# Performance work log

Measured on AMD Instinct MI355X. Metric: run time of the kernel, lower is better.

The kernel has to match this reference:

```python
import jax, jax.numpy as jnp
import numpy as np
import math

NUM_HEADS = 16
THETA = 10000.0


def _rope(x, token_pos, theta):
    # x: [B, H, S, d_k]; token_pos: [S]
    d_k = x.shape[-1]
    freqs = 1.0 / theta ** (jnp.arange(0, d_k, 2, dtype=jnp.float32) / d_k)  # [d_k/2]
    angles = token_pos.astype(jnp.float32)[:, None] * freqs[None, :]         # [S, d_k/2]
    cos, sin = jnp.cos(angles), jnp.sin(angles)
    x1 = x[..., 0::2]
    x2 = x[..., 1::2]
    out1 = x1 * cos - x2 * sin
    out2 = x1 * sin + x2 * cos
    # interleave back: (..., d_k/2, 2) -> (..., d_k)
    return jnp.stack([out1, out2], axis=-1).reshape(x.shape)


def setup_inputs() -> dict:
    key = jax.random.key(0)
    ks = jax.random.split(key, 5)
    B, S, D = 4, 2048, 1024
    scale = 0.02
    return {
        "x": jax.random.normal(ks[0], (B, S, D), dtype=jnp.float32),
        "token_pos": jnp.arange(S, dtype=jnp.int64 if jax.config.jax_enable_x64 else jnp.int32),
        "Wq": jax.random.normal(ks[1], (D, D), dtype=jnp.float32) * scale,
        "Wk": jax.random.normal(ks[2], (D, D), dtype=jnp.float32) * scale,
        "Wv": jax.random.normal(ks[3], (D, D), dtype=jnp.float32) * scale,
        "Wo": jax.random.normal(ks[4], (D, D), dtype=jnp.float32) * scale,
    }


def reference(x, token_pos, Wq, Wk, Wv, Wo):
    B, S, D = x.shape
    H = NUM_HEADS
    d_k = D // H
    # projections (Linear without bias: y = x @ W^T, W is [out, in])
    def proj(W):
        y = jnp.einsum('bsd,ed->bse', x, W)
        return y.reshape(B, S, H, d_k).transpose(0, 2, 1, 3)  # [B,H,S,d_k]
    q, k, v = proj(Wq), proj(Wk), proj(Wv)
    q = _rope(q, token_pos, THETA)
    k = _rope(k, token_pos, THETA)
    scores = jnp.einsum('bhqd,bhkd->bhqk', q, k) / math.sqrt(d_k)
    causal = jnp.tril(jnp.ones((S, S), dtype=bool))
    scores = jnp.where(causal, scores, -jnp.inf)
    attn = jax.nn.softmax(scores, axis=-1)
    out = jnp.einsum('bhqk,bhkd->bhqd', attn, v)            # [B,H,S,d_k]
    out = out.transpose(0, 2, 1, 3).reshape(B, S, D)
    return jnp.einsum('bsd,ed->bse', out, Wo)
```

## Files before the change

kernel.cpp:

```cpp
#include <hip/hip_runtime.h>

typedef unsigned short u16;
typedef __bf16 bf16x8 __attribute__((ext_vector_type(8)));
typedef float f32x4 __attribute__((ext_vector_type(4)));
typedef u16 u16x8 __attribute__((ext_vector_type(8)));

#define B_ 4
#define S_ 2048
#define D_ 1024
#define H_ 16
#define LOG2E 1.44269504f

__device__ inline u16 f2bf(float f) {
  unsigned u = __float_as_uint(f);
  u = u + 0x7fffu + ((u >> 16) & 1u);
  return (u16)(u >> 16);
}
__device__ inline u16 f2bf_hw(float f) {
  __bf16 b = (__bf16)f;
  return __builtin_bit_cast(u16, b);
}
__device__ inline float bf2f(u16 h) {
  return __uint_as_float(((unsigned)h) << 16);
}
__device__ inline void gload_lds16(const u16* g, u16* l) {
  __builtin_amdgcn_global_load_lds((const __attribute__((address_space(1))) void*)g,
                                   (__attribute__((address_space(3))) void*)l, 16, 0, 0);
}
__device__ inline float fast_exp2(float x) {
  float r;
  asm("v_exp_f32 %0, %1" : "=v"(r) : "v"(x));
  return r;
}

__global__ __launch_bounds__(256) void k_prep(const float* __restrict__ x,
                                              const float* __restrict__ w0,
                                              const float* __restrict__ w1,
                                              const float* __restrict__ w2,
                                              const float* __restrict__ w3,
                                              const int* __restrict__ pos,
                                              u16* __restrict__ xb,
                                              u16* __restrict__ wdst,
                                              float2* __restrict__ tab) {
  const int bid = blockIdx.x;
  if (bid < 8192) {
    int i = bid * 256 + threadIdx.x;
    float4 v = reinterpret_cast<const float4*>(x)[i];
    ushort4 o;
    o.x = f2bf(v.x); o.y = f2bf(v.y); o.z = f2bf(v.z); o.w = f2bf(v.w);
    reinterpret_cast<ushort4*>(xb)[i] = o;
  } else if (bid < 12288) {
    int i = (bid - 8192) * 256 + threadIdx.x;
    const int tensor = i >> 18;
    const int local = i & 262143;
    const float* s = tensor == 0 ? w0 : tensor == 1 ? w1 : tensor == 2 ? w2 : w3;
    float4 v = reinterpret_cast<const float4*>(s)[local];
    ushort4 o;
    o.x = f2bf(v.x); o.y = f2bf(v.y); o.z = f2bf(v.z); o.w = f2bf(v.w);
    reinterpret_cast<ushort4*>(wdst + (size_t)tensor * 1048576)[local] = o;
  } else {
    int idx = (bid - 12288) * 256 + threadIdx.x;
    int s = idx >> 5, i = idx & 31;
    float freq = powf(10000.0f, -(float)i * (1.0f / 32.0f));
    float ang = (float)pos[s] * freq;
    float sn, c;
    sincosf(ang, &sn, &c);
    tab[idx] = make_float2(c, sn);
  }
}

__global__ __launch_bounds__(256) void k_rope_k(u16* __restrict__ kb,
                                                const float2* __restrict__ tab) {
  int idx = blockIdx.x * 256 + threadIdx.x;
  const int row = idx >> 7;
  const int s = row & 2047;
  const int chunk = idx & 127;
  u16* p = kb + ((size_t)row << 10) + chunk * 8;
  u16x8 v = *reinterpret_cast<u16x8*>(p);
  const float4* tp = reinterpret_cast<const float4*>(tab + s * 32 + (chunk & 7) * 4);
  float4 t0 = tp[0], t1 = tp[1];
  float cc[4] = {t0.x, t0.z, t1.x, t1.z};
  float ss[4] = {t0.y, t0.w, t1.y, t1.w};
  u16x8 o;
#pragma unroll
  for (int u = 0; u < 4; u++) {
    float x1 = bf2f(v[2 * u]), x2 = bf2f(v[2 * u + 1]);
    o[2 * u]     = f2bf(x1 * cc[u] - x2 * ss[u]);
    o[2 * u + 1] = f2bf(x1 * ss[u] + x2 * cc[u]);
  }
  *reinterpret_cast<u16x8*>(p) = o;
}

__global__ __launch_bounds__(256) void k_gemm_qkv(const u16* __restrict__ A,
                                                  const u16* __restrict__ Bcat,
                                                  u16* __restrict__ Ccat,
                                                  u16* __restrict__ Vt) {
  __shared__ u16 As[2][128 * 64];
  __shared__ u16 Bs[2][128 * 64];
  const int K = 1024;
  const int xcd = blockIdx.x & 7;
  const int idx = blockIdx.x >> 3;
  const int st = idx >> 6;
  const int mi = (idx & 63) >> 3;
  const int ni = idx & 7;
  const int by = xcd * 8 + mi;
  const int bx = st * 8 + ni;
  const int m0 = by << 7, n0 = bx << 7;
  const int tid = threadIdx.x;
  const int lane = tid & 63;
  const int wv = tid >> 6;
  const int wm = (wv >> 1) << 6;
  const int wn = (wv & 1) << 6;
  const int r = lane & 15, g = lane >> 4;

  f32x4 acc[4][4] = {};

  const int srow0 = tid >> 3;
  const int scol = (((tid & 7) ^ ((tid >> 3) & 7)) * 8);
  const int csw = r & 7;

  const u16* Ab = A + (size_t)(m0 + srow0) * K + scol;
  const u16* Bb = Bcat + (size_t)(n0 + srow0) * K + scol;

#define STAGEQ(k0v, bf) do {                                       \
    const u16* a_ = Ab + (k0v);                                    \
    const u16* b_ = Bb + (k0v);                                    \
    gload_lds16(a_,                &As[bf][0] + tid * 8);          \
    gload_lds16(a_ + (size_t)32 * K, &As[bf][0] + tid * 8 + 2048); \
    gload_lds16(a_ + (size_t)64 * K, &As[bf][0] + tid * 8 + 4096); \
    gload_lds16(a_ + (size_t)96 * K, &As[bf][0] + tid * 8 + 6144); \
    gload_lds16(b_,                &Bs[bf][0] + tid * 8);          \
    gload_lds16(b_ + (size_t)32 * K, &Bs[bf][0] + tid * 8 + 2048); \
    gload_lds16(b_ + (size_t)64 * K, &Bs[bf][0] + tid * 8 + 4096); \
    gload_lds16(b_ + (size_t)96 * K, &Bs[bf][0] + tid * 8 + 6144); \
  } while (0)

  STAGEQ(0, 0);

  for (int t = 0; t < 16; ++t) {
    const int bsel = t & 1;
    if (t < 15) {
      STAGEQ((t + 1) * 64, bsel ^ 1);
      asm volatile("s_waitcnt vmcnt(8)" ::: "memory");
    } else {
      asm volatile("s_waitcnt vmcnt(0)" ::: "memory");
    }
    __builtin_amdgcn_s_barrier();
    asm volatile("" ::: "memory");

#pragma unroll
    for (int ks = 0; ks < 2; ks++) {
      bf16x8 af[4], bfr[4];
#pragma unroll
      for (int i = 0; i < 4; i++)
        af[i] = *reinterpret_cast<const bf16x8*>(
            &As[bsel][(wm + i * 16 + r) * 64 + (((ks * 4 + g) ^ csw) * 8)]);
#pragma unroll
      for (int t2 = 0; t2 < 4; t2++)
        bfr[t2] = *reinterpret_cast<const bf16x8*>(
            &Bs[bsel][(wn + t2 * 16 + r) * 64 + (((ks * 4 + g) ^ csw) * 8)]);
#pragma unroll
      for (int i = 0; i < 4; i++)
#pragma unroll
        for (int t2 = 0; t2 < 4; t2++)
          acc[i][t2] = __builtin_amdgcn_mfma_f32_16x16x32_bf16(af[i], bfr[t2], acc[i][t2], 0, 0, 0);
    }
    asm volatile("" ::: "memory");
    __builtin_amdgcn_s_barrier();
  }
#undef STAGEQ

  const int bq = n0 >> 10;
  const int c0 = n0 & 1023;
  if (bq == 2) {
#pragma unroll
    for (int i = 0; i < 4; i++) {
#pragma unroll
      for (int t = 0; t < 4; t++) {
        const int row = m0 + wm + i * 16 + g * 4;
        const int col = c0 + wn + t * 16 + r;
        const int b = row >> 11, s0 = row & 2047;
        const int h = col >> 6, d = col & 63;
        ushort4 o;
        o.x = f2bf(acc[i][t][0]); o.y = f2bf(acc[i][t][1]);
        o.z = f2bf(acc[i][t][2]); o.w = f2bf(acc[i][t][3]);
        *reinterpret_cast<ushort4*>(
            Vt + (((size_t)(b * 16 + h) * 64 + d) << 11) + s0) = o;
      }
    }
  } else {
    u16* Cb = Ccat + (size_t)bq * (8192 * 1024);
#pragma unroll
    for (int i = 0; i < 4; i++) {
#pragma unroll
      for (int t = 0; t < 4; t++) {
        const int row = m0 + wm + i * 16 + g * 4;
        const int col = c0 + wn + t * 16 + r;
#pragma unroll
        for (int j = 0; j < 4; j++)
          Cb[(size_t)(row + j) * 1024 + col] = f2bf(acc[i][t][j]);
      }
    }
  }
}

__global__ __launch_bounds__(256) void k_gemm_bt(const u16* __restrict__ A,
                                                 const u16* __restrict__ Bw,
                                                 float* __restrict__ C,
                                                 int M, int N, int K) {
  __shared__ u16 As[2][128 * 64];
  __shared__ u16 Bs[2][128 * 64];
  const int nbx = N >> 7;
  const int swz = (blockIdx.x & 7) * (gridDim.x >> 3) + (blockIdx.x >> 3);
  const int bx = swz % nbx;
  const int by = swz / nbx;
  const int m0 = by << 7, n0 = bx << 7;
  const int tid = threadIdx.x;
  const int lane = tid & 63;
  const int wv = tid >> 6;
  const int wm = (wv >> 1) << 6;
  const int wn = (wv & 1) << 6;
  const int r = lane & 15, g = lane >> 4;

  f32x4 acc[4][4] = {};

  const int srow0 = tid >> 3;
  const int scol = (((tid & 7) ^ ((tid >> 3) & 7)) * 8);
  const int csw = r & 7;

  const u16* Ab = A + (size_t)(m0 + srow0) * K + scol;
  const u16* Bb = Bw + (size_t)(n0 + srow0) * K + scol;
  const int nt = K >> 6;

#define STAGEW(k0v, bf) do {                                       \
    const u16* a_ = Ab + (k0v);                                    \
    const u16* b_ = Bb + (k0v);                                    \
    gload_lds16(a_,                &As[bf][0] + tid * 8);          \
    gload_lds16(a_ + (size_t)32 * K, &As[bf][0] + tid * 8 + 2048); \
    gload_lds16(a_ + (size_t)64 * K, &As[bf][0] + tid * 8 + 4096); \
    gload_lds16(a_ + (size_t)96 * K, &As[bf][0] + tid * 8 + 6144); \
    gload_lds16(b_,                &Bs[bf][0] + tid * 8);          \
    gload_lds16(b_ + (size_t)32 * K, &Bs[bf][0] + tid * 8 + 2048); \
    gload_lds16(b_ + (size_t)64 * K, &Bs[bf][0] + tid * 8 + 4096); \
    gload_lds16(b_ + (size_t)96 * K, &Bs[bf][0] + tid * 8 + 6144); \
  } while (0)

  STAGEW(0, 0);

  for (int t = 0; t < nt; ++t) {
    const int bsel = t & 1;
    if (t < nt - 1) {
      STAGEW((t + 1) * 64, bsel ^ 1);
      asm volatile("s_waitcnt vmcnt(8)" ::: "memory");
    } else {
      asm volatile("s_waitcnt vmcnt(0)" ::: "memory");
    }
    __builtin_amdgcn_s_barrier();
    asm volatile("" ::: "memory");

#pragma unroll
    for (int ks = 0; ks < 2; ks++) {
      bf16x8 af[4], bfr[4];
#pragma unroll
      for (int i = 0; i < 4; i++)
        af[i] = *reinterpret_cast<const bf16x8*>(
            &As[bsel][(wm + i * 16 + r) * 64 + (((ks * 4 + g) ^ csw) * 8)]);
#pragma unroll
      for (int t2 = 0; t2 < 4; t2++)
        bfr[t2] = *reinterpret_cast<const bf16x8*>(
            &Bs[bsel][(wn + t2 * 16 + r) * 64 + (((ks * 4 + g) ^ csw) * 8)]);
#pragma unroll
      for (int i = 0; i < 4; i++)
#pragma unroll
        for (int t2 = 0; t2 < 4; t2++)
          acc[i][t2] = __builtin_amdgcn_mfma_f32_16x16x32_bf16(af[i], bfr[t2], acc[i][t2], 0, 0, 0);
    }
    asm volatile("" ::: "memory");
    __builtin_amdgcn_s_barrier();
  }
#undef STAGEW

#pragma unroll
  for (int i = 0; i < 4; i++) {
#pragma unroll
    for (int t = 0; t < 4; t++) {
      const int row = m0 + wm + i * 16 + g * 4;
      const int col = n0 + wn + t * 16 + r;
#pragma unroll
      for (int j = 0; j < 4; j++)
        C[(size_t)(row + j) * N + col] = acc[i][t][j];
    }
  }
}

__global__ __launch_bounds__(256) void k_attn14(const u16* __restrict__ Q,
                                                const u16* __restrict__ Kb,
                                                const u16* __restrict__ Vt,
                                                const float2* __restrict__ tab,
                                                u16* __restrict__ O) {
  __shared__ u16 Ks[64 * 64];
  __shared__ u16 Vs[64 * 64];
  __shared__ u16 Ps[4][32 * 64];

  const int bh = (blockIdx.x & 7) * 8 + ((blockIdx.x >> 3) & 7);
  const int qt = 15 - (blockIdx.x >> 6);
  const int b = bh >> 4, h = bh & 15;
  const int tid = threadIdx.x;
  const int lane = tid & 63, w = tid >> 6;
  const int g = lane >> 4, r = lane & 15;

  const u16* Kbase = Kb + (size_t)(b * S_) * 1024 + h * 64;
  const u16* Vbase = Vt + (size_t)bh * 64 * 2048;

  const int srow = tid >> 3;
  const int scol = ((tid & 7) * 8) ^ ((srow & 7) * 8);
  const int rsw = (r & 7) * 8;

  const int qbase = qt << 7;
  const int qrow0 = qbase + (w << 5);

  const float QSC = 0.125f * LOG2E;
  bf16x8 qf[2][2];
#pragma unroll
  for (int f = 0; f < 2; f++) {
    const int s = qrow0 + f * 16 + r;
    const u16* qrow = Q + (size_t)(b * S_ + s) * 1024 + h * 64;
    qf[f][0] = *reinterpret_cast<const bf16x8*>(qrow + g * 8);
    qf[f][1] = *reinterpret_cast<const bf16x8*>(qrow + 32 + g * 8);
    const float4* tp = reinterpret_cast<const float4*>(tab + s * 32);
#pragma unroll
    for (int c = 0; c < 2; c++) {
      float4 t0 = tp[c * 8 + g * 2], t1 = tp[c * 8 + g * 2 + 1];
      float cc[4] = {t0.x, t0.z, t1.x, t1.z};
      float ss[4] = {t0.y, t0.w, t1.y, t1.w};
      bf16x8 q = qf[f][c];
#pragma unroll
      for (int u = 0; u < 4; u++) {
        float x1 = (float)q[2 * u], x2 = (float)q[2 * u + 1];
        q[2 * u]     = (__bf16)((x1 * cc[u] - x2 * ss[u]) * QSC);
        q[2 * u + 1] = (__bf16)((x1 * ss[u] + x2 * cc[u]) * QSC);
      }
      qf[f][c] = q;
    }
  }

  bf16x8 ones;
#pragma unroll
  for (int u = 0; u < 8; u++) ones[u] = (__bf16)1.0f;

  f32x4 o_acc[2][4] = {};
  f32x4 lacc[2] = {};
  u16* pb0 = &Ps[w][r * 64];
  u16* pb1 = &Ps[w][(16 + r) * 64];

  const u16* kp0 = Kbase + (size_t)srow * 1024 + scol;
  const u16* kp1 = kp0 + 32 * 1024;
  const u16* vp0 = Vbase + (size_t)srow * 2048 + scol;
  const u16* vp1 = vp0 + 32 * 2048;

  const int kend = qbase + 128;
  for (int k0 = 0; k0 < kend; k0 += 64) {
    gload_lds16(kp0, Ks + tid * 8);
    gload_lds16(kp1, Ks + tid * 8 + 2048);
    gload_lds16(vp0, Vs + tid * 8);
    gload_lds16(vp1, Vs + tid * 8 + 2048);
    kp0 += 64 * 1024; kp1 += 64 * 1024; vp0 += 64; vp1 += 64;
    __syncthreads();

    if (k0 <= qrow0 + 31) {
      const int rem0 = qrow0 + 15 - k0;
      const int rem1 = qrow0 + 31 - k0;
      const int ktlim0 = rem0 < 0 ? 0 : (rem0 >= 48 ? 4 : (rem0 >> 4) + 1);
      const int ktlim1 = rem1 >= 48 ? 4 : (rem1 >> 4) + 1;
      const bool mask0 = (k0 + 63 > qrow0);
      const bool mask1 = (k0 + 63 > qrow0 + 16);

#pragma unroll
      for (int kt = 0; kt < 4; kt++) {
        const int pc = (kt * 16 + g * 4) ^ rsw;
        if (kt >= ktlim1) {
          ushort4 z = {0, 0, 0, 0};
          *reinterpret_cast<ushort4*>(pb0 + pc) = z;
          *reinterpret_cast<ushort4*>(pb1 + pc) = z;
          continue;
        }
        const int krow = kt * 16 + r;
        bf16x8 kf0 = *reinterpret_cast<const bf16x8*>(&Ks[krow * 64 + ((g * 8) ^ rsw)]);
        bf16x8 kf1 = *reinterpret_cast<const bf16x8*>(&Ks[krow * 64 + ((32 + g * 8) ^ rsw)]);
        f32x4 s0 = {}, s1 = {};
        if (kt < ktlim0) {
          s0 = __builtin_amdgcn_mfma_f32_16x16x32_bf16(kf0, qf[0][0], s0, 0, 0, 0);
          s0 = __builtin_amdgcn_mfma_f32_16x16x32_bf16(kf1, qf[0][1], s0, 0, 0, 0);
        }
        s1 = __builtin_amdgcn_mfma_f32_16x16x32_bf16(kf0, qf[1][0], s1, 0, 0, 0);
        s1 = __builtin_amdgcn_mfma_f32_16x16x32_bf16(kf1, qf[1][1], s1, 0, 0, 0);

        const int colb = k0 + kt * 16 + g * 4;
        float p0[4], p1[4];
        if (kt < ktlim0) {
          if (mask0) {
#pragma unroll
            for (int j = 0; j < 4; j++)
              if (colb + j > qrow0 + r) s0[j] = -1e30f;
          }
#pragma unroll
          for (int j = 0; j < 4; j++) p0[j] = fast_exp2(s0[j]);
        } else {
#pragma unroll
          for (int j = 0; j < 4; j++) p0[j] = 0.f;
        }
        if (mask1) {
#pragma unroll
          for (int j = 0; j < 4; j++)
            if (colb + j > qrow0 + 16 + r) s1[j] = -1e30f;
        }
#pragma unroll
        for (int j = 0; j < 4; j++) p1[j] = fast_exp2(s1[j]);

        ushort4 w0, w1;
        w0.x = f2bf_hw(p0[0]); w0.y = f2bf_hw(p0[1]); w0.z = f2bf_hw(p0[2]); w0.w = f2bf_hw(p0[3]);
        w1.x = f2bf_hw(p1[0]); w1.y = f2bf_hw(p1[1]); w1.z = f2bf_hw(p1[2]); w1.w = f2bf_hw(p1[3]);
        *reinterpret_cast<ushort4*>(pb0 + pc) = w0;
        *reinterpret_cast<ushort4*>(pb1 + pc) = w1;
      }
      asm volatile("s_waitcnt lgkmcnt(0)" ::: "memory");

#pragma unroll
      for (int kc = 0; kc < 2; kc++) {
        const int cb = (kc * 32 + g * 8) ^ rsw;
        bf16x8 pf0 = *reinterpret_cast<const bf16x8*>(pb0 + cb);
        bf16x8 pf1 = *reinterpret_cast<const bf16x8*>(pb1 + cb);
        lacc[0] = __builtin_amdgcn_mfma_f32_16x16x32_bf16(pf0, ones, lacc[0], 0, 0, 0);
        lacc[1] = __builtin_amdgcn_mfma_f32_16x16x32_bf16(pf1, ones, lacc[1], 0, 0, 0);
#pragma unroll
        for (int dt = 0; dt < 4; dt++) {
          bf16x8 vf = *reinterpret_cast<const bf16x8*>(
              &Vs[(dt * 16 + r) * 64 + ((kc * 32 + g * 8) ^ rsw)]);
          o_acc[0][dt] = __builtin_amdgcn_mfma_f32_16x16x32_bf16(pf0, vf, o_acc[0][dt], 0, 0, 0);
          o_acc[1][dt] = __builtin_amdgcn_mfma_f32_16x16x32_bf16(pf1, vf, o_acc[1][dt], 0, 0, 0);
        }
      }
    }
    __syncthreads();
  }

#pragma unroll
  for (int f = 0; f < 2; f++) {
    u16* orow = O + (size_t)(b * S_ + qrow0 + f * 16) * 1024 + h * 64;
#pragma unroll
    for (int j = 0; j < 4; j++) {
      const float rln = 1.0f / lacc[f][j];
#pragma unroll
      for (int dt = 0; dt < 4; dt++)
        orow[(size_t)(g * 4 + j) * 1024 + dt * 16 + r] = f2bf(o_acc[f][dt][j] * rln);
    }
  }
}

extern "C" void kernel_launch(void* const* d_in, const int* in_sizes, int n_in,
                              void* d_out, int out_size, void* d_ws, size_t ws_size,
                              hipStream_t stream) {
  const float* x  = (const float*)d_in[0];
  const int*   pos = (const int*)d_in[1];
  const float* Wq = (const float*)d_in[2];
  const float* Wk = (const float*)d_in[3];
  const float* Wv = (const float*)d_in[4];
  const float* Wo = (const float*)d_in[5];
  float* out = (float*)d_out;

  char* ws = (char*)d_ws;
  size_t off = 0;
  auto alloc = [&](size_t bytes) {
    void* p = ws + off;
    off += (bytes + 255) & ~(size_t)255;
    return p;
  };
  const size_t XB = (size_t)8192 * 1024 * 2;
  u16* xb  = (u16*)alloc(XB);
  u16* wqb = (u16*)alloc((size_t)1024 * 1024 * 2);
  u16* wkb = (u16*)alloc((size_t)1024 * 1024 * 2);
  u16* wvb = (u16*)alloc((size_t)1024 * 1024 * 2);
  u16* wob = (u16*)alloc((size_t)1024 * 1024 * 2);
  u16* qb  = (u16*)alloc(XB);
  u16* kb  = (u16*)alloc(XB);
  u16* ob  = (u16*)alloc(XB);
  u16* vt  = (u16*)alloc(XB);
  float2* tab = (float2*)alloc((size_t)2048 * 32 * sizeof(float2));
  (void)wkb; (void)wvb;

  k_prep<<<12544, 256, 0, stream>>>(x, Wq, Wk, Wv, Wo, pos, xb, wqb, tab);

  k_gemm_qkv<<<1536, 256, 0, stream>>>(xb, wqb, qb, vt);

  k_rope_k<<<4096, 256, 0, stream>>>(kb, tab);

  k_attn14<<<1024, 256, 0, stream>>>(qb, kb, vt, tab, ob);

  k_gemm_bt<<<512, 256, 0, stream>>>(ob, wob, out, 8192, 1024, 1024);
}
```

Baseline: 171.6 us.

## Widen QKV GEMM tile to 128x256 and drop double-buffered LDS pipeline

The QKV projection GEMM now computes 128x256 output tiles per block, with each wave holding a 64x128 accumulator. The grid is halved and the block-to-tile mapping is rewritten. The double-buffered async-load pipeline with explicit vmcnt waits is replaced by a single-buffered loop that loads and then syncs, so global loads no longer overlap with MFMA work. The aim is more arithmetic per loaded byte and fewer blocks, at the cost of exposed load latency, higher register pressure (128 accumulator floats per thread), and possibly lower occupancy.

Result: slower. 197.2 us (+14.9%).

```diff
diff --git a/kernel.cpp b/kernel.cpp
--- a/kernel.cpp
+++ b/kernel.cpp
@@ -95,25 +95,23 @@
                                                   const u16* __restrict__ Bcat,
                                                   u16* __restrict__ Ccat,
                                                   u16* __restrict__ Vt) {
-  __shared__ u16 As[2][128 * 64];
-  __shared__ u16 Bs[2][128 * 64];
+  __shared__ u16 As[128 * 64];
+  __shared__ u16 Bs[256 * 64];
   const int K = 1024;
   const int xcd = blockIdx.x & 7;
   const int idx = blockIdx.x >> 3;
-  const int st = idx >> 6;
-  const int mi = (idx & 63) >> 3;
-  const int ni = idx & 7;
-  const int by = xcd * 8 + mi;
-  const int bx = st * 8 + ni;
-  const int m0 = by << 7, n0 = bx << 7;
+  const int win = idx >> 5;
+  const int by = xcd * 8 + ((idx >> 2) & 7);
+  const int bx = win * 4 + (idx & 3);
+  const int m0 = by << 7, n0 = bx << 8;
   const int tid = threadIdx.x;
   const int lane = tid & 63;
   const int wv = tid >> 6;
   const int wm = (wv >> 1) << 6;
-  const int wn = (wv & 1) << 6;
+  const int wn = (wv & 1) << 7;
   const int r = lane & 15, g = lane >> 4;
 
-  f32x4 acc[4][4] = {};
+  f32x4 acc[4][8] = {};
 
   const int srow0 = tid >> 3;
   const int scol = (((tid & 7) ^ ((tid >> 3) & 7)) * 8);
@@ -122,53 +120,34 @@
   const u16* Ab = A + (size_t)(m0 + srow0) * K + scol;
   const u16* Bb = Bcat + (size_t)(n0 + srow0) * K + scol;
 
-#define STAGEQ(k0v, bf) do {                                       \
-    const u16* a_ = Ab + (k0v);                                    \
-    const u16* b_ = Bb + (k0v);                                    \
-    gload_lds16(a_,                &As[bf][0] + tid * 8);          \
-    gload_lds16(a_ + (size_t)32 * K, &As[bf][0] + tid * 8 + 2048); \
-    gload_lds16(a_ + (size_t)64 * K, &As[bf][0] + tid * 8 + 4096); \
-    gload_lds16(a_ + (size_t)96 * K, &As[bf][0] + tid * 8 + 6144); \
-    gload_lds16(b_,                &Bs[bf][0] + tid * 8);          \
-    gload_lds16(b_ + (size_t)32 * K, &Bs[bf][0] + tid * 8 + 2048); \
-    gload_lds16(b_ + (size_t)64 * K, &Bs[bf][0] + tid * 8 + 4096); \
-    gload_lds16(b_ + (size_t)96 * K, &Bs[bf][0] + tid * 8 + 6144); \
-  } while (0)
-
-  STAGEQ(0, 0);
-
-  for (int t = 0; t < 16; ++t) {
-    const int bsel = t & 1;
-    if (t < 15) {
-      STAGEQ((t + 1) * 64, bsel ^ 1);
-      asm volatile("s_waitcnt vmcnt(8)" ::: "memory");
-    } else {
-      asm volatile("s_waitcnt vmcnt(0)" ::: "memory");
-    }
-    __builtin_amdgcn_s_barrier();
-    asm volatile("" ::: "memory");
+  for (int k0 = 0; k0 < K; k0 += 64) {
+#pragma unroll
+    for (int i = 0; i < 4; i++)
+      gload_lds16(Ab + k0 + (size_t)(32 * i) * K, As + tid * 8 + i * 2048);
+#pragma unroll
+    for (int i = 0; i < 8; i++)
+      gload_lds16(Bb + k0 + (size_t)(32 * i) * K, Bs + tid * 8 + i * 2048);
+    __syncthreads();
 
 #pragma unroll
     for (int ks = 0; ks < 2; ks++) {
-      bf16x8 af[4], bfr[4];
+      bf16x8 af[4], bfr[8];
 #pragma unroll
       for (int i = 0; i < 4; i++)
         af[i] = *reinterpret_cast<const bf16x8*>(
-            &As[bsel][(wm + i * 16 + r) * 64 + (((ks * 4 + g) ^ csw) * 8)]);
-#pragma unroll
-      for (int t2 = 0; t2 < 4; t2++)
+            &As[(wm + i * 16 + r) * 64 + (((ks * 4 + g) ^ csw) * 8)]);
+#pragma unroll
+      for (int t2 = 0; t2 < 8; t2++)
         bfr[t2] = *reinterpret_cast<const bf16x8*>(
-            &Bs[bsel][(wn + t2 * 16 + r) * 64 + (((ks * 4 + g) ^ csw) * 8)]);
+            &Bs[(wn + t2 * 16 + r) * 64 + (((ks * 4 + g) ^ csw) * 8)]);
 #pragma unroll
       for (int i = 0; i < 4; i++)
 #pragma unroll
-        for (int t2 = 0; t2 < 4; t2++)
+        for (int t2 = 0; t2 < 8; t2++)
           acc[i][t2] = __builtin_amdgcn_mfma_f32_16x16x32_bf16(af[i], bfr[t2], acc[i][t2], 0, 0, 0);
     }
-    asm volatile("" ::: "memory");
-    __builtin_amdgcn_s_barrier();
-  }
-#undef STAGEQ
+    __syncthreads();
+  }
 
   const int bq = n0 >> 10;
   const int c0 = n0 & 1023;
@@ -176,7 +155,7 @@
 #pragma unroll
     for (int i = 0; i < 4; i++) {
 #pragma unroll
-      for (int t = 0; t < 4; t++) {
+      for (int t = 0; t < 8; t++) {
         const int row = m0 + wm + i * 16 + g * 4;
         const int col = c0 + wn + t * 16 + r;
         const int b = row >> 11, s0 = row & 2047;
@@ -193,7 +172,7 @@
 #pragma unroll
     for (int i = 0; i < 4; i++) {
 #pragma unroll
-      for (int t = 0; t < 4; t++) {
+      for (int t = 0; t < 8; t++) {
         const int row = m0 + wm + i * 16 + g * 4;
         const int col = c0 + wn + t * 16 + r;
 #pragma unroll
@@ -490,7 +469,7 @@
 
   k_prep<<<12544, 256, 0, stream>>>(x, Wq, Wk, Wv, Wo, pos, xb, wqb, tab);
 
-  k_gemm_qkv<<<1536, 256, 0, stream>>>(xb, wqb, qb, vt);
+  k_gemm_qkv<<<768, 256, 0, stream>>>(xb, wqb, qb, vt);
 
   k_rope_k<<<4096, 256, 0, stream>>>(kb, tab);
 
```

## Split fused QKV GEMM into 256x256-tile QK GEMM and separate V GEMM

Applied to the files above, without the earlier changes.

Replaces the single 128x128-tile QKV projection kernel with two launches. Q and K are computed by a new 512-thread kernel using 256x256 tiles, which gives more data reuse per LDS load and fewer blocks. V is computed by its own 128x128 kernel that writes the transposed layout. This adds an extra launch and a tail effect (256 blocks on 256 CUs, one wave) in exchange for higher arithmetic intensity on the QK part. It also doubles LDS per block (64KB) and raises register pressure from 32 accumulator tiles per wave.

Result: faster. 167.2 us (median of 3 runs) (-2.6%).

```diff
diff --git a/kernel.cpp b/kernel.cpp
--- a/kernel.cpp
+++ b/kernel.cpp
@@ -91,20 +91,103 @@
   *reinterpret_cast<u16x8*>(p) = o;
 }
 
-__global__ __launch_bounds__(256) void k_gemm_qkv(const u16* __restrict__ A,
-                                                  const u16* __restrict__ Bcat,
-                                                  u16* __restrict__ Ccat,
-                                                  u16* __restrict__ Vt) {
+__global__ __launch_bounds__(512) void k_gemm_qk(const u16* __restrict__ A,
+                                                 const u16* __restrict__ Bqk,
+                                                 u16* __restrict__ Cqk) {
+  __shared__ u16 As[2][256 * 64];
+  __shared__ u16 Bs[2][256 * 64];
+  const int K = 1024;
+  const int xcd = blockIdx.x & 7;
+  const int idx = blockIdx.x >> 3;
+  const int by = xcd * 4 + (idx & 3);
+  const int bx = idx >> 2;
+  const int m0 = by << 8, n0 = bx << 8;
+  const int tid = threadIdx.x;
+  const int lane = tid & 63, w = tid >> 6;
+  const int wr = w >> 2, wc = w & 3;
+  const int r = lane & 15, g = lane >> 4;
+
+  f32x4 acc[8][4] = {};
+
+  const int srow = tid >> 3;
+  const int scol = (((tid & 7) ^ ((tid >> 3) & 7)) * 8);
+  const int csw = r & 7;
+
+  const u16* Ab = A + (size_t)(m0 + srow) * K + scol;
+  const u16* Bb = Bqk + (size_t)(n0 + srow) * K + scol;
+
+#define STG(k0v, bf) do {                                                \
+    gload_lds16(Ab + (k0v),                   &As[bf][0] + tid * 8);     \
+    gload_lds16(Ab + (k0v) + (size_t)64 * K,  &As[bf][0] + tid * 8 + 4096);  \
+    gload_lds16(Ab + (k0v) + (size_t)128 * K, &As[bf][0] + tid * 8 + 8192);  \
+    gload_lds16(Ab + (k0v) + (size_t)192 * K, &As[bf][0] + tid * 8 + 12288); \
+    gload_lds16(Bb + (k0v),                   &Bs[bf][0] + tid * 8);     \
+    gload_lds16(Bb + (k0v) + (size_t)64 * K,  &Bs[bf][0] + tid * 8 + 4096);  \
+    gload_lds16(Bb + (k0v) + (size_t)128 * K, &Bs[bf][0] + tid * 8 + 8192);  \
+    gload_lds16(Bb + (k0v) + (size_t)192 * K, &Bs[bf][0] + tid * 8 + 12288); \
+  } while (0)
+
+  STG(0, 0);
+
+  for (int t = 0; t < 16; ++t) {
+    const int bsel = t & 1;
+    if (t < 15) {
+      STG((t + 1) * 64, bsel ^ 1);
+      asm volatile("s_waitcnt vmcnt(8)" ::: "memory");
+    } else {
+      asm volatile("s_waitcnt vmcnt(0)" ::: "memory");
+    }
+    __builtin_amdgcn_s_barrier();
+    asm volatile("" ::: "memory");
+
+    const u16* Ah = &As[bsel][(wr * 128) * 64];
+    const u16* Bh = &Bs[bsel][(wc * 64) * 64];
+#pragma unroll
+    for (int ks = 0; ks < 2; ks++) {
+      bf16x8 bfr[4];
+#pragma unroll
+      for (int t2 = 0; t2 < 4; t2++)
+        bfr[t2] = *reinterpret_cast<const bf16x8*>(
+            &Bh[(t2 * 16 + r) * 64 + (((ks * 4 + g) ^ csw) * 8)]);
+#pragma unroll
+      for (int i = 0; i < 8; i++) {
+        bf16x8 af = *reinterpret_cast<const bf16x8*>(
+            &Ah[(i * 16 + r) * 64 + (((ks * 4 + g) ^ csw) * 8)]);
+#pragma unroll
+        for (int t2 = 0; t2 < 4; t2++)
+          acc[i][t2] = __builtin_amdgcn_mfma_f32_16x16x32_bf16(af, bfr[t2], acc[i][t2], 0, 0, 0);
+      }
+    }
+    asm volatile("" ::: "memory");
+    __builtin_amdgcn_s_barrier();
+  }
+#undef STG
+
+  u16* Cb = Cqk + (size_t)(n0 >> 10) * (8192 * 1024);
+  const int c0 = n0 & 1023;
+#pragma unroll
+  for (int i = 0; i < 8; i++) {
+#pragma unroll
+    for (int t2 = 0; t2 < 4; t2++) {
+      const int row = m0 + wr * 128 + i * 16 + g * 4;
+      const int col = c0 + wc * 64 + t2 * 16 + r;
+#pragma unroll
+      for (int j = 0; j < 4; j++)
+        Cb[(size_t)(row + j) * 1024 + col] = f2bf(acc[i][t2][j]);
+    }
+  }
+}
+
+__global__ __launch_bounds__(256) void k_gemm_v(const u16* __restrict__ A,
+                                                const u16* __restrict__ Bw,
+                                                u16* __restrict__ Vt) {
   __shared__ u16 As[2][128 * 64];
   __shared__ u16 Bs[2][128 * 64];
   const int K = 1024;
   const int xcd = blockIdx.x & 7;
   const int idx = blockIdx.x >> 3;
-  const int st = idx >> 6;
-  const int mi = (idx & 63) >> 3;
-  const int ni = idx & 7;
-  const int by = xcd * 8 + mi;
-  const int bx = st * 8 + ni;
+  const int by = xcd * 8 + (idx & 7);
+  const int bx = idx >> 3;
   const int m0 = by << 7, n0 = bx << 7;
   const int tid = threadIdx.x;
   const int lane = tid & 63;
@@ -120,9 +203,9 @@
   const int csw = r & 7;
 
   const u16* Ab = A + (size_t)(m0 + srow0) * K + scol;
-  const u16* Bb = Bcat + (size_t)(n0 + srow0) * K + scol;
-
-#define STAGEQ(k0v, bf) do {                                       \
+  const u16* Bb = Bw + (size_t)(n0 + srow0) * K + scol;
+
+#define STAGEV(k0v, bf) do {                                       \
     const u16* a_ = Ab + (k0v);                                    \
     const u16* b_ = Bb + (k0v);                                    \
     gload_lds16(a_,                &As[bf][0] + tid * 8);          \
@@ -135,12 +218,12 @@
     gload_lds16(b_ + (size_t)96 * K, &Bs[bf][0] + tid * 8 + 6144); \
   } while (0)
 
-  STAGEQ(0, 0);
+  STAGEV(0, 0);
 
   for (int t = 0; t < 16; ++t) {
     const int bsel = t & 1;
     if (t < 15) {
-      STAGEQ((t + 1) * 64, bsel ^ 1);
+      STAGEV((t + 1) * 64, bsel ^ 1);
       asm volatile("s_waitcnt vmcnt(8)" ::: "memory");
     } else {
       asm volatile("s_waitcnt vmcnt(0)" ::: "memory");
@@ -168,38 +251,21 @@
     asm volatile("" ::: "memory");
     __builtin_amdgcn_s_barrier();
   }
-#undef STAGEQ
-
-  const int bq = n0 >> 10;
-  const int c0 = n0 & 1023;
-  if (bq == 2) {
-#pragma unroll
-    for (int i = 0; i < 4; i++) {
-#pragma unroll
-      for (int t = 0; t < 4; t++) {
-        const int row = m0 + wm + i * 16 + g * 4;
-        const int col = c0 + wn + t * 16 + r;
-        const int b = row >> 11, s0 = row & 2047;
-        const int h = col >> 6, d = col & 63;
-        ushort4 o;
-        o.x = f2bf(acc[i][t][0]); o.y = f2bf(acc[i][t][1]);
-        o.z = f2bf(acc[i][t][2]); o.w = f2bf(acc[i][t][3]);
-        *reinterpret_cast<ushort4*>(
-            Vt + (((size_t)(b * 16 + h) * 64 + d) << 11) + s0) = o;
-      }
-    }
-  } else {
-    u16* Cb = Ccat + (size_t)bq * (8192 * 1024);
-#pragma unroll
-    for (int i = 0; i < 4; i++) {
-#pragma unroll
-      for (int t = 0; t < 4; t++) {
-        const int row = m0 + wm + i * 16 + g * 4;
-        const int col = c0 + wn + t * 16 + r;
-#pragma unroll
-        for (int j = 0; j < 4; j++)
-          Cb[(size_t)(row + j) * 1024 + col] = f2bf(acc[i][t][j]);
-      }
+#undef STAGEV
+
+#pragma unroll
+  for (int i = 0; i < 4; i++) {
+#pragma unroll
+    for (int t = 0; t < 4; t++) {
+      const int row = m0 + wm + i * 16 + g * 4;
+      const int col = n0 + wn + t * 16 + r;
+      const int b = row >> 11, s0 = row & 2047;
+      const int h = col >> 6, d = col & 63;
+      ushort4 o;
+      o.x = f2bf(acc[i][t][0]); o.y = f2bf(acc[i][t][1]);
+      o.z = f2bf(acc[i][t][2]); o.w = f2bf(acc[i][t][3]);
+      *reinterpret_cast<ushort4*>(
+          Vt + (((size_t)(b * 16 + h) * 64 + d) << 11) + s0) = o;
     }
   }
 }
@@ -486,11 +552,13 @@
   u16* ob  = (u16*)alloc(XB);
   u16* vt  = (u16*)alloc(XB);
   float2* tab = (float2*)alloc((size_t)2048 * 32 * sizeof(float2));
-  (void)wkb; (void)wvb;
+  (void)wkb;
 
   k_prep<<<12544, 256, 0, stream>>>(x, Wq, Wk, Wv, Wo, pos, xb, wqb, tab);
 
-  k_gemm_qkv<<<1536, 256, 0, stream>>>(xb, wqb, qb, vt);
+  k_gemm_qk<<<256, 512, 0, stream>>>(xb, wqb, qb);
+
+  k_gemm_v<<<512, 256, 0, stream>>>(xb, wvb, vt);
 
   k_rope_k<<<4096, 256, 0, stream>>>(kb, tab);
 
```
